# Performance work log

Measured on AMD Instinct MI355X. Metric: run time of the kernel, lower is better.

The kernel has to match this reference:

```python
import jax, jax.numpy as jnp
import numpy as np

E = 200      # embsize
R = 480      # num relations
T = 8        # cur_ts (history length)
N = 40000    # num entities
B = 1024     # batch of triples
NEG_INF = -1.0e9


def _lin(x, W, b):
    # torch nn.Linear convention: y = x @ W.T + b
    return x @ W.T + b


def _gru_cell(x, h, wih, whh, bih, bhh):
    # torch GRUCell: gates packed as [r, z, n]
    gi = x @ wih.T + bih
    gh = h @ whh.T + bhh
    i_r, i_z, i_n = jnp.split(gi, 3, axis=1)
    h_r, h_z, h_n = jnp.split(gh, 3, axis=1)
    r = jax.nn.sigmoid(i_r + h_r)
    z = jax.nn.sigmoid(i_z + h_z)
    n = jnp.tanh(i_n + r * h_n)
    return (1.0 - z) * n + z * h


def setup_inputs() -> dict:
    key = jax.random.key(0)
    ks = jax.random.split(key, 24)
    s = 0.05
    pre_emb = jax.random.normal(ks[0], (N, E), dtype=jnp.float32)
    r_emb = jax.random.normal(ks[1], (R, E), dtype=jnp.float32)
    partial_embeding = jax.random.randint(ks[2], (B, T * R), 0, 2).astype(jnp.float32)
    sub = jax.random.randint(ks[3], (B,), 0, N)
    rel = jax.random.randint(ks[4], (B,), 0, R)
    obj = jax.random.randint(ks[5], (B,), 0, N)
    all_triples = jnp.stack([sub, rel, obj], axis=1).astype(jnp.int64)
    params = {
        'W1': jax.random.normal(ks[6], (2 * E, E)) * s, 'b1': jnp.zeros((2 * E,)),
        'W2': jax.random.normal(ks[7], (E, 2 * E)) * s, 'b2': jnp.zeros((E,)),
        'Wa': jax.random.normal(ks[8], (E, E)) * s, 'ba': jnp.zeros((E,)),
        'Wh1': jax.random.normal(ks[9], (E, E)) * s, 'bh1': jnp.zeros((E,)),
        'Wh2': jax.random.normal(ks[10], (E, E)) * s, 'bh2': jnp.zeros((E,)),
        'Wal': jax.random.normal(ks[11], (E, E)) * s, 'bal': jnp.zeros((E,)),
        'gru_wih': jax.random.normal(ks[12], (3 * E, E)) * s,
        'gru_whh': jax.random.normal(ks[13], (3 * E, E)) * s,
        'gru_bih': jnp.zeros((3 * E,)),
        'gru_bhh': jnp.zeros((3 * E,)),
    }
    params = {k: v.astype(jnp.float32) for k, v in params.items()}
    out = {'pre_emb': pre_emb, 'r_emb': r_emb, 'partial_embeding': partial_embeding,
           'all_triples': all_triples, 'cur_ts': T, 'num_rel': R}
    out.update(params)
    return out


def reference(pre_emb, r_emb, partial_embeding, all_triples, cur_ts, num_rel,
              W1, b1, W2, b2, Wa, ba, Wh1, bh1, Wh2, bh2, Wal, bal,
              gru_wih, gru_whh, gru_bih, gru_bhh):
    mapped_rel = _lin(_lin(r_emb, W1, b1), W2, b2)          # [R, E]
    q_rel = mapped_rel[all_triples[:, 1]]                    # [B, E]
    b = partial_embeding.shape[0]

    # loop-invariant attention base: linear_attn(q_rel) @ mapped_rel^T -> [B, R]
    base = _lin(q_rel, Wa, ba) @ mapped_rel.T

    # [B, cur_ts*R] -> [cur_ts, B, R] for scan over timesteps
    pe = partial_embeding.reshape(b, cur_ts, num_rel).transpose(1, 0, 2)

    def step(h, cur):
        attn = cur * base
        attn = jnp.where(attn == 0, jnp.float32(NEG_INF), attn)
        a = jax.nn.softmax(attn, axis=1)
        x = a @ mapped_rel                                   # [B, E]
        h = _gru_cell(x, h, gru_wih, gru_whh, gru_bih, gru_bhh)
        return h, None

    h0 = jnp.zeros((b, mapped_rel.shape[1]), dtype=pre_emb.dtype)
    gru_hidden, _ = jax.lax.scan(step, h0, pe)

    predicted_hist = 0.1 * _lin(_lin(q_rel, Wh1, bh1), Wh2, bh2) + q_rel
    match_loss = jnp.mean((predicted_hist - gru_hidden) ** 2)

    # forward_forth (distmult scoring)
    gru_hidden2 = _gru_cell(q_rel, predicted_hist, gru_wih, gru_whh, gru_bih, gru_bhh)
    sub_emb = pre_emb[all_triples[:, 0]]
    score_logits = (_lin(sub_emb, Wal, bal) * gru_hidden2) @ _lin(pre_emb, Wal, bal).T  # [B, N]
    score = jax.nn.sigmoid(score_logits)

    labels = jnp.zeros_like(score_logits).at[jnp.arange(b), all_triples[:, 2]].set(1.0)
    # stable BCE(sigmoid(s), y)
    path_loss = -jnp.mean(labels * jax.nn.log_sigmoid(score_logits)
                          + (1.0 - labels) * jax.nn.log_sigmoid(-score_logits))
    return (match_loss, path_loss, score)
```

## Files before the change

### kernel.cpp

```cpp
#include <hip/hip_runtime.h>
#include <hip/hip_bf16.h>
#include <math.h>

#define EE 200
#define RR 480
#define TT 8
#define NN 40000
#define BB 1024
#define KP 224
#define GP 672
#define GPR 704
#define LDS_STRIDE 232

typedef __attribute__((ext_vector_type(8))) short short8v;
typedef __attribute__((ext_vector_type(4))) float f32x4;

__device__ inline unsigned short f2bf(float x) {
    unsigned int u = __float_as_uint(x);
    unsigned int r = ((u >> 16) & 1u) + 0x7fffu;
    return (unsigned short)((u + r) >> 16);
}
__device__ inline float bf2f(unsigned short h) {
    return __uint_as_float(((unsigned int)h) << 16);
}
__device__ inline float sigm(float x) { return 1.0f / (1.0f + __expf(-x)); }
__device__ inline void split_store(unsigned short* hi, unsigned short* lo, size_t i, float v) {
    unsigned short h = f2bf(v);
    hi[i] = h;
    lo[i] = f2bf(v - bf2f(h));
}

struct PrepPtrs {
    unsigned short *W1h, *W1l, *W2h, *W2l, *Wabh, *Wabl, *Wh2h, *Wh2l;
    unsigned short *Walh, *Wall, *WTh, *WTl, *wgh, *wgl, *whg, *whl;
    float *bab, *bihp, *bhhp;
    unsigned short *mapSh, *mapSl, *wgiSh, *wgiSl, *hbufs;
    double* acc;
};

__global__ __launch_bounds__(256) void prep_kernel(
    const float* __restrict__ W1, const float* __restrict__ W2,
    const float* __restrict__ Wa, const float* __restrict__ Wh1,
    const float* __restrict__ Wh2, const float* __restrict__ Wal,
    const float* __restrict__ bal, const float* __restrict__ wih,
    const float* __restrict__ whh, const float* __restrict__ ba,
    const float* __restrict__ bh1, const float* __restrict__ bih,
    const float* __restrict__ bhh, PrepPtrs p)
{
    const int gt = blockIdx.x * 256 + threadIdx.x;
    const int gs = gridDim.x * 256;

    for (int i = gt; i < 448 * 224; i += gs) {
        int r = i / 224, c = i - r * 224;
        split_store(p.W1h, p.W1l, i, (r < 400 && c < 200) ? W1[r * 200 + c] : 0.f);
        float vab = 0.f;
        if (c < 200) {
            if (r < 200) vab = Wa[r * 200 + c];
            else if (r >= 224 && r < 424) vab = Wh1[(r - 224) * 200 + c];
        }
        split_store(p.Wabh, p.Wabl, i, vab);
    }
    for (int i = gt; i < 256 * 416; i += gs) {
        int r = i / 416, c = i - r * 416;
        split_store(p.W2h, p.W2l, i, (r < 200 && c < 400) ? W2[r * 400 + c] : 0.f);
    }
    for (int i = gt; i < 256 * 224; i += gs) {
        int r = i / 224, c = i - r * 224;
        bool in = (r < 200 && c < 200);
        split_store(p.Wh2h, p.Wh2l, i, in ? Wh2[r * 200 + c] : 0.f);
        split_store(p.Walh, p.Wall, i, in ? Wal[r * 200 + c] : 0.f);
        float vt = in ? Wal[c * 200 + r] : ((r == 200 && c < 200) ? bal[c] : 0.f);
        split_store(p.WTh, p.WTl, i, vt);
    }
    for (int i = gt; i < 672 * 224; i += gs) {
        int rr = i / 224, c = i - rr * 224;
        int g = rr / 224, j = rr - g * 224;
        bool in = (j < 200 && c < 200);
        split_store(p.wgh, p.wgl, i, in ? wih[(size_t)(g * 200 + j) * 200 + c] : 0.f);
        split_store(p.whg, p.whl, i, in ? whh[(size_t)(g * 200 + j) * 200 + c] : 0.f);
    }
    for (int i = gt; i < 448; i += gs) {
        float v = 0.f;
        if (i < 200) v = ba[i];
        else if (i >= 224 && i < 424) v = bh1[i - 224];
        p.bab[i] = v;
    }
    for (int i = gt; i < GPR; i += gs) {
        int g = i / 224, j = i - g * 224;
        p.bihp[i] = (g < 3 && j < 200) ? bih[g * 200 + j] : 0.f;
    }
    for (int i = gt; i < GP; i += gs) {
        int g = i / 224, j = i - g * 224;
        p.bhhp[i] = (j < 200) ? bhh[g * 200 + j] : 0.f;
    }
    for (int i = gt; i < 512 * 224; i += gs) { p.mapSh[i] = 0; p.mapSl[i] = 0; }
    for (int i = gt; i < 704 * 480; i += gs) { p.wgiSh[i] = 0; p.wgiSl[i] = 0; }
    for (int i = gt; i < 4 * BB * KP; i += gs) p.hbufs[i] = 0;
    if (gt == 0) { p.acc[0] = 0.0; p.acc[1] = 0.0; }
}

template <int MODE, int OUT, int GATHER, int GATEPAD, int EGATHER>
__global__ __launch_bounds__(256) void mfma_flyA(
    const float* __restrict__ A, int lda, const int* __restrict__ gidx, int gsel,
    const unsigned short* __restrict__ Bhi, const unsigned short* __restrict__ Blo,
    const float* __restrict__ bias,
    float* __restrict__ Cf, unsigned short* __restrict__ Chi, unsigned short* __restrict__ Clo,
    int M, int N, int Ka, int Ks,
    const float* __restrict__ extra, int eld, float alpha, int obf)
{
    const int tid = threadIdx.x;
    const int wave = tid >> 6, lane = tid & 63;
    const int r16 = lane & 15, kq = lane >> 4;
    const int kbase = kq * 8;
    const int bm = blockIdx.y * 64 + wave * 16;
    const int bn = blockIdx.x * 64;

    int arow = bm + r16;
    const bool avalid = arow < M;
    if (GATHER) { if (avalid) arow = gidx[arow * 3 + gsel]; }
    const float* Ap = A + (size_t)arow * lda;

    f32x4 acc[4] = {{0,0,0,0},{0,0,0,0},{0,0,0,0},{0,0,0,0}};
    const int nk = Ks >> 5;

    for (int kk = 0; kk < nk; kk++) {
        const int k0 = kk * 32 + kbase;
        short8v a0, a1;
        #pragma unroll
        for (int e = 0; e < 8; e++) {
            float v = (avalid && (k0 + e) < Ka) ? Ap[k0 + e] : 0.f;
            unsigned short h = f2bf(v);
            a0[e] = (short)h;
            a1[e] = (short)f2bf(v - bf2f(h));
        }
        #pragma unroll
        for (int nf = 0; nf < 4; nf++) {
            const size_t boff = (size_t)(bn + nf * 16 + r16) * Ks + k0;
            short8v b0 = *(const short8v*)(Bhi + boff);
            short8v b1 = *(const short8v*)(Blo + boff);
            acc[nf] = __builtin_amdgcn_mfma_f32_16x16x32_bf16(a0, b1, acc[nf], 0, 0, 0);
            acc[nf] = __builtin_amdgcn_mfma_f32_16x16x32_bf16(a1, b0, acc[nf], 0, 0, 0);
            acc[nf] = __builtin_amdgcn_mfma_f32_16x16x32_bf16(a0, b0, acc[nf], 0, 0, 0);
        }
    }

    #pragma unroll
    for (int r = 0; r < 4; r++) {
        const int orow = bm + kq * 4 + r;
        if (orow >= M) continue;
        #pragma unroll
        for (int nf = 0; nf < 4; nf++) {
            const int col = bn + nf * 16 + r16;
            float v = acc[nf][r];
            if (OUT == 0) {
                if (col < N) {
                    if (bias) v += bias[col];
                    if (MODE == 1) {
                        float ex = EGATHER ? extra[(size_t)gidx[orow * 3 + gsel] * eld + col]
                                           : extra[(size_t)orow * eld + col];
                        v = alpha * v + ex;
                    } else if (MODE == 2) {
                        v = v * extra[(size_t)orow * eld + col];
                    }
                    Cf[(size_t)orow * N + col] = v;
                }
            } else if (OUT == 1) {
                if (col < obf) {
                    float w = 0.f;
                    if (col < N) { w = v; if (bias) w += bias[col]; }
                    Chi[(size_t)orow * obf + col] = f2bf(w);
                }
            } else if (OUT == 2) {
                if (col < N) {
                    int wr = GATEPAD ? (orow / 200) * 224 + orow % 200 : orow;
                    if (bias) v += bias[col];
                    split_store(Chi, Clo, (size_t)wr * obf + col, v);
                }
            } else if (OUT == 3) {
                if (col < N) {
                    if (bias) v += bias[col];
                    Cf[(size_t)orow * N + col] = v;
                    split_store(Chi, Clo, (size_t)orow * obf + col, v);
                }
            }
        }
    }
}

__global__ __launch_bounds__(256) void mfma_linear1_kernel(
    const unsigned short* __restrict__ Ahi,
    const unsigned short* __restrict__ Bhi,
    const float* __restrict__ bias, float* __restrict__ C,
    int M, int N, int Ks)
{
    const int tid  = threadIdx.x;
    const int wave = tid >> 6;
    const int lane = tid & 63;
    const int r16   = lane & 15;
    const int khalf = lane >> 4;
    const int kbase = khalf * 8;
    const int bm = blockIdx.y * 64 + wave * 16;
    const int bn = blockIdx.x * 64;

    const unsigned short* ah = Ahi + (size_t)(bm + r16) * Ks + kbase;
    const unsigned short* bh = Bhi + (size_t)(bn + r16) * Ks + kbase;

    f32x4 acc[4] = {{0,0,0,0},{0,0,0,0},{0,0,0,0},{0,0,0,0}};

    for (int k0 = 0; k0 < Ks; k0 += 32) {
        short8v a0 = *(const short8v*)(ah + k0);
        #pragma unroll
        for (int nf = 0; nf < 4; nf++) {
            short8v b0 = *(const short8v*)(bh + (size_t)nf * 16 * Ks + k0);
            acc[nf] = __builtin_amdgcn_mfma_f32_16x16x32_bf16(a0, b0, acc[nf], 0, 0, 0);
        }
    }
    #pragma unroll
    for (int r = 0; r < 4; r++) {
        const int row = bm + khalf * 4 + r;
        #pragma unroll
        for (int nf = 0; nf < 4; nf++) {
            const int col = bn + nf * 16 + r16;
            if (col < N)
                C[(size_t)row * N + col] = acc[nf][r] + (bias ? bias[col] : 0.0f);
        }
    }
}

template <int FIRST, int LAST>
__global__ __launch_bounds__(256) void gru_step_kernel(
    const unsigned short* __restrict__ Whi, const unsigned short* __restrict__ Wlo,
    const float* __restrict__ bhh_pad,
    const float* __restrict__ gi_t,
    const unsigned short* __restrict__ hin_hi, const unsigned short* __restrict__ hin_lo,
    unsigned short* __restrict__ hout_hi, unsigned short* __restrict__ hout_lo,
    float* __restrict__ h_fin)
{
    const int tid = threadIdx.x;
    const int wave = tid >> 6, lane = tid & 63;
    const int r16 = lane & 15, kq = lane >> 4;
    const int jf = blockIdx.x;
    const int brow = (blockIdx.y * 4 + wave) * 16;
    const int j = jf * 16 + r16;

    f32x4 ar = {0,0,0,0}, az = {0,0,0,0}, an = {0,0,0,0};
    if (!FIRST) {
        short8v ahi[7], alo[7];
        const unsigned short* hh = hin_hi + (size_t)(brow + r16) * KP + kq * 8;
        const unsigned short* hl = hin_lo + (size_t)(brow + r16) * KP + kq * 8;
        #pragma unroll
        for (int kk = 0; kk < 7; kk++) {
            ahi[kk] = *(const short8v*)(hh + kk * 32);
            alo[kk] = *(const short8v*)(hl + kk * 32);
        }
        #pragma unroll
        for (int kk = 0; kk < 7; kk++) {
            const size_t rowr = (size_t)(jf * 16 + r16) * KP + kk * 32 + kq * 8;
            const size_t rowz = rowr + (size_t)224 * KP;
            const size_t rown = rowr + (size_t)448 * KP;
            short8v brh = *(const short8v*)(Whi + rowr);
            short8v brl = *(const short8v*)(Wlo + rowr);
            short8v bzh = *(const short8v*)(Whi + rowz);
            short8v bzl = *(const short8v*)(Wlo + rowz);
            short8v bnh = *(const short8v*)(Whi + rown);
            short8v bnl = *(const short8v*)(Wlo + rown);
            ar = __builtin_amdgcn_mfma_f32_16x16x32_bf16(ahi[kk], brl, ar, 0, 0, 0);
            az = __builtin_amdgcn_mfma_f32_16x16x32_bf16(ahi[kk], bzl, az, 0, 0, 0);
            an = __builtin_amdgcn_mfma_f32_16x16x32_bf16(ahi[kk], bnl, an, 0, 0, 0);
            ar = __builtin_amdgcn_mfma_f32_16x16x32_bf16(alo[kk], brh, ar, 0, 0, 0);
            az = __builtin_amdgcn_mfma_f32_16x16x32_bf16(alo[kk], bzh, az, 0, 0, 0);
            an = __builtin_amdgcn_mfma_f32_16x16x32_bf16(alo[kk], bnh, an, 0, 0, 0);
            ar = __builtin_amdgcn_mfma_f32_16x16x32_bf16(ahi[kk], brh, ar, 0, 0, 0);
            az = __builtin_amdgcn_mfma_f32_16x16x32_bf16(ahi[kk], bzh, az, 0, 0, 0);
            an = __builtin_amdgcn_mfma_f32_16x16x32_bf16(ahi[kk], bnh, an, 0, 0, 0);
        }
    }

    const float br = bhh_pad[j], bz = bhh_pad[224 + j], bn_ = bhh_pad[448 + j];
    #pragma unroll
    for (int q = 0; q < 4; q++) {
        const int row = brow + kq * 4 + q;
        float gir = gi_t[(size_t)row * GP + j];
        float giz = gi_t[(size_t)row * GP + 224 + j];
        float gin = gi_t[(size_t)row * GP + 448 + j];
        float r_ = sigm(gir + ar[q] + br);
        float z_ = sigm(giz + az[q] + bz);
        float n_ = tanhf(gin + r_ * (an[q] + bn_));
        float hold = 0.0f;
        if (!FIRST)
            hold = bf2f(hin_hi[(size_t)row * KP + j]) + bf2f(hin_lo[(size_t)row * KP + j]);
        float hnew = (1.0f - z_) * n_ + z_ * hold;
        if (j < EE) {
            unsigned short nh = f2bf(hnew);
            hout_hi[(size_t)row * KP + j] = nh;
            hout_lo[(size_t)row * KP + j] = f2bf(hnew - bf2f(nh));
            if (LAST) h_fin[(size_t)row * EE + j] = hnew;
        }
    }
}

__global__ __launch_bounds__(256) void gru2_fused_kernel(
    const unsigned short* __restrict__ Wihi, const unsigned short* __restrict__ Wilo,
    const unsigned short* __restrict__ Whhi, const unsigned short* __restrict__ Whlo,
    const float* __restrict__ bih_pad, const float* __restrict__ bhh_pad,
    const int* __restrict__ triples, const float* __restrict__ map,
    const float* __restrict__ hp, const float* __restrict__ hfin,
    float* __restrict__ ghid2, double* __restrict__ accMatch)
{
    __shared__ float red[256];
    const int tid = threadIdx.x;
    const int wave = tid >> 6, lane = tid & 63;
    const int r16 = lane & 15, kq = lane >> 4;
    const int jf = blockIdx.x;
    const int brow = (blockIdx.y * 4 + wave) * 16;
    const int j = jf * 16 + r16;

    f32x4 ir = {0,0,0,0}, iz = {0,0,0,0}, in_ = {0,0,0,0};
    f32x4 hr = {0,0,0,0}, hz = {0,0,0,0}, hn = {0,0,0,0};

    {
        const int xrow = triples[(brow + r16) * 3 + 1];
        const float* xp = map + (size_t)xrow * EE;
        #pragma unroll
        for (int kk = 0; kk < 7; kk++) {
            short8v a0, a1;
            #pragma unroll
            for (int e = 0; e < 8; e++) {
                int k = kk * 32 + kq * 8 + e;
                float v = (k < EE) ? xp[k] : 0.0f;
                unsigned short hhh = f2bf(v);
                a0[e] = (short)hhh;
                a1[e] = (short)f2bf(v - bf2f(hhh));
            }
            const size_t rowr = (size_t)(jf * 16 + r16) * KP + kk * 32 + kq * 8;
            const size_t rowz = rowr + (size_t)224 * KP;
            const size_t rown = rowr + (size_t)448 * KP;
            short8v brh = *(const short8v*)(Wihi + rowr);
            short8v brl = *(const short8v*)(Wilo + rowr);
            short8v bzh = *(const short8v*)(Wihi + rowz);
            short8v bzl = *(const short8v*)(Wilo + rowz);
            short8v bnh = *(const short8v*)(Wihi + rown);
            short8v bnl = *(const short8v*)(Wilo + rown);
            ir = __builtin_amdgcn_mfma_f32_16x16x32_bf16(a0, brl, ir, 0, 0, 0);
            iz = __builtin_amdgcn_mfma_f32_16x16x32_bf16(a0, bzl, iz, 0, 0, 0);
            in_ = __builtin_amdgcn_mfma_f32_16x16x32_bf16(a0, bnl, in_, 0, 0, 0);
            ir = __builtin_amdgcn_mfma_f32_16x16x32_bf16(a1, brh, ir, 0, 0, 0);
            iz = __builtin_amdgcn_mfma_f32_16x16x32_bf16(a1, bzh, iz, 0, 0, 0);
            in_ = __builtin_amdgcn_mfma_f32_16x16x32_bf16(a1, bnh, in_, 0, 0, 0);
            ir = __builtin_amdgcn_mfma_f32_16x16x32_bf16(a0, brh, ir, 0, 0, 0);
            iz = __builtin_amdgcn_mfma_f32_16x16x32_bf16(a0, bzh, iz, 0, 0, 0);
            in_ = __builtin_amdgcn_mfma_f32_16x16x32_bf16(a0, bnh, in_, 0, 0, 0);
        }
    }
    {
        const float* hpp = hp + (size_t)(brow + r16) * EE;
        #pragma unroll
        for (int kk = 0; kk < 7; kk++) {
            short8v a0, a1;
            #pragma unroll
            for (int e = 0; e < 8; e++) {
                int k = kk * 32 + kq * 8 + e;
                float v = (k < EE) ? hpp[k] : 0.0f;
                unsigned short hhh = f2bf(v);
                a0[e] = (short)hhh;
                a1[e] = (short)f2bf(v - bf2f(hhh));
            }
            const size_t rowr = (size_t)(jf * 16 + r16) * KP + kk * 32 + kq * 8;
            const size_t rowz = rowr + (size_t)224 * KP;
            const size_t rown = rowr + (size_t)448 * KP;
            short8v brh = *(const short8v*)(Whhi + rowr);
            short8v brl = *(const short8v*)(Whlo + rowr);
            short8v bzh = *(const short8v*)(Whhi + rowz);
            short8v bzl = *(const short8v*)(Whlo + rowz);
            short8v bnh = *(const short8v*)(Whhi + rown);
            short8v bnl = *(const short8v*)(Whlo + rown);
            hr = __builtin_amdgcn_mfma_f32_16x16x32_bf16(a0, brl, hr, 0, 0, 0);
            hz = __builtin_amdgcn_mfma_f32_16x16x32_bf16(a0, bzl, hz, 0, 0, 0);
            hn = __builtin_amdgcn_mfma_f32_16x16x32_bf16(a0, bnl, hn, 0, 0, 0);
            hr = __builtin_amdgcn_mfma_f32_16x16x32_bf16(a1, brh, hr, 0, 0, 0);
            hz = __builtin_amdgcn_mfma_f32_16x16x32_bf16(a1, bzh, hz, 0, 0, 0);
            hn = __builtin_amdgcn_mfma_f32_16x16x32_bf16(a1, bnh, hn, 0, 0, 0);
            hr = __builtin_amdgcn_mfma_f32_16x16x32_bf16(a0, brh, hr, 0, 0, 0);
            hz = __builtin_amdgcn_mfma_f32_16x16x32_bf16(a0, bzh, hz, 0, 0, 0);
            hn = __builtin_amdgcn_mfma_f32_16x16x32_bf16(a0, bnh, hn, 0, 0, 0);
        }
    }

    float psum = 0.0f;
    if (j < EE) {
        const float bir = bih_pad[j], biz = bih_pad[224 + j], bin = bih_pad[448 + j];
        const float bhr = bhh_pad[j], bhz = bhh_pad[224 + j], bhn = bhh_pad[448 + j];
        #pragma unroll
        for (int q = 0; q < 4; q++) {
            const int row = brow + kq * 4 + q;
            float r_ = sigm(ir[q] + bir + hr[q] + bhr);
            float z_ = sigm(iz[q] + biz + hz[q] + bhz);
            float n_ = tanhf(in_[q] + bin + r_ * (hn[q] + bhn));
            float hold = hp[(size_t)row * EE + j];
            ghid2[(size_t)row * EE + j] = (1.0f - z_) * n_ + z_ * hold;
            float d = hold - hfin[(size_t)row * EE + j];
            psum += d * d;
        }
    }
    red[tid] = psum;
    __syncthreads();
    for (int s = 128; s > 0; s >>= 1) {
        if (tid < s) red[tid] += red[tid + s];
        __syncthreads();
    }
    if (tid == 0) atomicAdd(accMatch, (double)red[0]);
}

__global__ __launch_bounds__(256) void score_mfma2_kernel(
    const unsigned short* __restrict__ Ubf,
    const float* __restrict__ pre_emb,
    const int* __restrict__ triples,
    float* __restrict__ outScore,
    double* __restrict__ accPath)
{
    __shared__ unsigned short Bs[32 * LDS_STRIDE];
    __shared__ int objs[BB];
    __shared__ float red[256];

    const int tid = threadIdx.x;
    const int bn = blockIdx.x * 32;

    for (int i = tid; i < BB; i += 256) objs[i] = triples[i * 3 + 2];

    for (int idx = tid; idx < 32 * 50; idx += 256) {
        int row = idx / 50;
        int c4 = (idx - row * 50) * 4;
        float4 v = *(const float4*)(pre_emb + (size_t)(bn + row) * EE + c4);
        unsigned short* d = &Bs[row * LDS_STRIDE + c4];
        d[0] = f2bf(v.x); d[1] = f2bf(v.y); d[2] = f2bf(v.z); d[3] = f2bf(v.w);
    }
    for (int idx = tid; idx < 32 * 24; idx += 256) {
        int row = idx / 24;
        int cc = idx - row * 24;
        Bs[row * LDS_STRIDE + 200 + cc] = (cc == 0) ? (unsigned short)0x3F80 : (unsigned short)0;
    }
    __syncthreads();

    const int wave  = tid >> 6;
    const int lane  = tid & 63;
    const int r16   = lane & 15;
    const int khalf = lane >> 4;
    const int kbase = khalf * 8;

    short8v b0r[7], b1r[7];
    #pragma unroll
    for (int kk = 0; kk < 7; kk++) {
        b0r[kk] = *(const short8v*)&Bs[( 0 + r16) * LDS_STRIDE + kk * 32 + kbase];
        b1r[kk] = *(const short8v*)&Bs[(16 + r16) * LDS_STRIDE + kk * 32 + kbase];
    }

    float psum = 0.0f;

    for (int mi = 0; mi < 16; mi++) {
        const int m0 = mi * 64 + wave * 16;
        const unsigned short* Ap = Ubf + (size_t)(m0 + r16) * KP + kbase;
        f32x4 acc0 = {0,0,0,0}, acc1 = {0,0,0,0};
        #pragma unroll
        for (int kk = 0; kk < 7; kk++) {
            short8v a = *(const short8v*)(Ap + kk * 32);
            acc0 = __builtin_amdgcn_mfma_f32_16x16x32_bf16(a, b0r[kk], acc0, 0, 0, 0);
            acc1 = __builtin_amdgcn_mfma_f32_16x16x32_bf16(a, b1r[kk], acc1, 0, 0, 0);
        }
        #pragma unroll
        for (int r = 0; r < 4; r++) {
            const int grow = m0 + khalf * 4 + r;
            const int objc = objs[grow];
            float xv[2] = { acc0[r], acc1[r] };
            #pragma unroll
            for (int nf = 0; nf < 2; nf++) {
                const int col = bn + nf * 16 + r16;
                float x  = xv[nf];
                float e  = __expf(-fabsf(x));
                float t1 = 1.0f + e;
                float rc = __builtin_amdgcn_rcpf(t1);
                float sig = (x >= 0.0f) ? rc : e * rc;
                float sp = __logf(t1);
                float s  = (col == objc) ? x : -x;
                psum += fminf(s, 0.0f) - sp;
                outScore[(size_t)grow * NN + col] = sig;
            }
        }
    }
    red[tid] = psum;
    __syncthreads();
    for (int s = 128; s > 0; s >>= 1) {
        if (tid < s) red[tid] += red[tid + s];
        __syncthreads();
    }
    if (tid == 0) atomicAdd(accPath, (double)red[0]);
}

__global__ __launch_bounds__(256) void masked_softmax_all_kernel(
    const float* __restrict__ base, const float* __restrict__ part,
    unsigned short* __restrict__ aout_hi)
{
    __shared__ float sv[RR];
    __shared__ float red[256];
    const int blk = blockIdx.x;
    const int b = blk & (BB - 1);
    const int t = blk >> 10;
    const int tid = threadIdx.x;
    const float* brow = base + (size_t)b * RR;
    const float* prow = part + (size_t)b * (TT * RR) + t * RR;

    float lmax = -3.0e38f;
    for (int r = tid; r < RR; r += 256) {
        float v = prow[r] * brow[r];
        if (v == 0.0f) v = -1000000000.0f;
        sv[r] = v;
        lmax = fmaxf(lmax, v);
    }
    red[tid] = lmax;
    __syncthreads();
    for (int s = 128; s > 0; s >>= 1) {
        if (tid < s) red[tid] = fmaxf(red[tid], red[tid + s]);
        __syncthreads();
    }
    float gmax = red[0];
    __syncthreads();

    float lsum = 0.0f;
    for (int r = tid; r < RR; r += 256) {
        float e = __expf(sv[r] - gmax);
        sv[r] = e;
        lsum += e;
    }
    red[tid] = lsum;
    __syncthreads();
    for (int s = 128; s > 0; s >>= 1) {
        if (tid < s) red[tid] += red[tid + s];
        __syncthreads();
    }
    float inv = 1.0f / red[0];
    for (int r = tid; r < RR; r += 256)
        aout_hi[(size_t)blk * RR + r] = f2bf(sv[r] * inv);
}

__global__ void final_kernel(const double* __restrict__ acc, float* __restrict__ out)
{
    if (threadIdx.x == 0) {
        out[0] = (float)(acc[0] / ((double)BB * EE));
        out[1] = (float)(-acc[1] / ((double)BB * NN));
    }
}

extern "C" void kernel_launch(void* const* d_in, const int* in_sizes, int n_in,
                              void* d_out, int out_size, void* d_ws, size_t ws_size,
                              hipStream_t stream) {
    const float* pre_emb = (const float*)d_in[0];
    const float* r_emb   = (const float*)d_in[1];
    const float* part    = (const float*)d_in[2];
    const int*   triples = (const int*)d_in[3];
    const float* W1  = (const float*)d_in[6];
    const float* b1  = (const float*)d_in[7];
    const float* W2  = (const float*)d_in[8];
    const float* b2  = (const float*)d_in[9];
    const float* Wa  = (const float*)d_in[10];
    const float* ba  = (const float*)d_in[11];
    const float* Wh1 = (const float*)d_in[12];
    const float* bh1 = (const float*)d_in[13];
    const float* Wh2 = (const float*)d_in[14];
    const float* bh2 = (const float*)d_in[15];
    const float* Wal = (const float*)d_in[16];
    const float* bal = (const float*)d_in[17];
    const float* wih = (const float*)d_in[18];
    const float* whh = (const float*)d_in[19];
    const float* bih = (const float*)d_in[20];
    const float* bhh = (const float*)d_in[21];

    float* out = (float*)d_out;
    double* acc = (double*)d_ws;
    float* wsf = (float*)d_ws;
    size_t off = 4;
    auto alloc = [&](size_t n) { float* p = wsf + off; off += (n + 3) & ~(size_t)3; return p; };
    auto allocS = [&](size_t n) { return (unsigned short*)alloc((n + 1) / 2); };

    PrepPtrs p;
    p.W1h  = allocS((size_t)448 * 224);
    p.W1l  = allocS((size_t)448 * 224);
    p.W2h  = allocS((size_t)256 * 416);
    p.W2l  = allocS((size_t)256 * 416);
    p.Wabh = allocS((size_t)448 * 224);
    p.Wabl = allocS((size_t)448 * 224);
    p.Wh2h = allocS((size_t)256 * 224);
    p.Wh2l = allocS((size_t)256 * 224);
    p.Walh = allocS((size_t)256 * 224);
    p.Wall = allocS((size_t)256 * 224);
    p.WTh  = allocS((size_t)256 * 224);
    p.WTl  = allocS((size_t)256 * 224);
    p.wgh  = allocS((size_t)GP * KP);
    p.wgl  = allocS((size_t)GP * KP);
    p.whg  = allocS((size_t)GP * KP);
    p.whl  = allocS((size_t)GP * KP);
    p.bab  = alloc(448);
    p.bihp = alloc(GPR);
    p.bhhp = alloc(GP);
    p.mapSh = allocS((size_t)512 * 224);
    p.mapSl = allocS((size_t)512 * 224);
    p.wgiSh = allocS((size_t)GPR * RR);
    p.wgiSl = allocS((size_t)GPR * RR);
    p.hbufs = allocS((size_t)4 * BB * KP);
    p.acc = acc;

    unsigned short* ha_hi = p.hbufs;
    unsigned short* ha_lo = p.hbufs + (size_t)BB * KP;
    unsigned short* hb_hi = p.hbufs + (size_t)2 * BB * KP;
    unsigned short* hb_lo = p.hbufs + (size_t)3 * BB * KP;

    float* h1     = alloc((size_t)RR * 400);
    float* map    = alloc((size_t)RR * EE);
    float* qa_ph1 = alloc((size_t)BB * 448);
    float* basep  = alloc((size_t)BB * RR);
    unsigned short* aw_hi = allocS((size_t)TT * BB * RR);
    float* gi_all = alloc((size_t)TT * BB * GP);
    float* hfin   = alloc((size_t)BB * EE);
    float* pred   = alloc((size_t)BB * EE);
    float* ghid2  = alloc((size_t)BB * EE);
    float* s1h    = alloc((size_t)BB * EE);
    unsigned short* u_bf = allocS((size_t)BB * KP);

    dim3 blk(256);

    prep_kernel<<<1024, blk, 0, stream>>>(
        W1, W2, Wa, Wh1, Wh2, Wal, bal, wih, whh, ba, bh1, bih, bhh, p);

    mfma_flyA<0,0,0,0,0><<<dim3(7, 8), blk, 0, stream>>>(
        r_emb, 200, nullptr, 0, p.W1h, p.W1l, b1, h1, nullptr, nullptr,
        RR, 400, 200, 224, nullptr, 0, 0.f, 0);
    mfma_flyA<0,3,0,0,0><<<dim3(4, 8), blk, 0, stream>>>(
        h1, 400, nullptr, 0, p.W2h, p.W2l, b2, map, p.mapSh, p.mapSl,
        RR, EE, 400, 416, nullptr, 0, 0.f, 224);
    mfma_flyA<0,0,1,0,0><<<dim3(7, 16), blk, 0, stream>>>(
        map, 200, triples, 1, p.Wabh, p.Wabl, p.bab, qa_ph1, nullptr, nullptr,
        BB, 448, 200, 224, nullptr, 0, 0.f, 0);
    mfma_flyA<0,0,0,0,0><<<dim3(8, 16), blk, 0, stream>>>(
        qa_ph1, 448, nullptr, 0, p.mapSh, p.mapSl, nullptr, basep, nullptr, nullptr,
        BB, RR, 200, 224, nullptr, 0, 0.f, 0);
    masked_softmax_all_kernel<<<TT * BB, blk, 0, stream>>>(basep, part, aw_hi);
    mfma_flyA<0,2,0,1,0><<<dim3(8, 10), blk, 0, stream>>>(
        wih, 200, nullptr, 0, p.mapSh, p.mapSl, nullptr, nullptr, p.wgiSh, p.wgiSl,
        600, RR, 200, 224, nullptr, 0, 0.f, RR);
    mfma_linear1_kernel<<<dim3(11, TT * BB / 64), blk, 0, stream>>>(
        aw_hi, p.wgiSh, p.bihp, gi_all, TT * BB, GP, RR);

    for (int t = 0; t < TT; t++) {
        const float* gi_t = gi_all + (size_t)t * BB * GP;
        const unsigned short* ih = (t & 1) ? hb_hi : ha_hi;
        const unsigned short* il = (t & 1) ? hb_lo : ha_lo;
        unsigned short* oh = (t & 1) ? ha_hi : hb_hi;
        unsigned short* ol = (t & 1) ? ha_lo : hb_lo;
        if (t == 0)
            gru_step_kernel<1,0><<<dim3(13, BB / 64), blk, 0, stream>>>(
                p.whg, p.whl, p.bhhp, gi_t, ih, il, oh, ol, nullptr);
        else if (t == TT - 1)
            gru_step_kernel<0,1><<<dim3(13, BB / 64), blk, 0, stream>>>(
                p.whg, p.whl, p.bhhp, gi_t, ih, il, oh, ol, hfin);
        else
            gru_step_kernel<0,0><<<dim3(13, BB / 64), blk, 0, stream>>>(
                p.whg, p.whl, p.bhhp, gi_t, ih, il, oh, ol, nullptr);
    }

    mfma_flyA<1,0,0,0,1><<<dim3(4, 16), blk, 0, stream>>>(
        qa_ph1 + 224, 448, triples, 1, p.Wh2h, p.Wh2l, bh2, pred, nullptr, nullptr,
        BB, EE, 200, 224, map, 200, 0.1f, 0);
    gru2_fused_kernel<<<dim3(13, BB / 64), blk, 0, stream>>>(
        p.wgh, p.wgl, p.whg, p.whl, p.bihp, p.bhhp,
        triples, map, pred, hfin, ghid2, acc + 0);
    mfma_flyA<2,0,1,0,0><<<dim3(4, 16), blk, 0, stream>>>(
        pre_emb, 200, triples, 0, p.Walh, p.Wall, bal, s1h, nullptr, nullptr,
        BB, EE, 200, 224, ghid2, 200, 0.f, 0);
    mfma_flyA<0,1,0,0,0><<<dim3(4, 16), blk, 0, stream>>>(
        s1h, 200, nullptr, 0, p.WTh, p.WTl, nullptr, nullptr, u_bf, nullptr,
        BB, KP, 200, 224, nullptr, 0, 0.f, KP);
    score_mfma2_kernel<<<NN / 32, blk, 0, stream>>>(u_bf, pre_emb, triples, out + 2, acc + 1);
    final_kernel<<<1, 64, 0, stream>>>(acc, out);
}
```

Before: 400.5 us.

## Restructure score GEMM grid to keep A fragments in registers and stream entity tiles

```diff
diff --git a/kernel.cpp b/kernel.cpp
--- a/kernel.cpp
+++ b/kernel.cpp
@@ -11,6 +11,7 @@
 #define GP 672
 #define GPR 704
 #define LDS_STRIDE 232
+#define SPAN 800
 
 typedef __attribute__((ext_vector_type(8))) short short8v;
 typedef __attribute__((ext_vector_type(4))) float f32x4;
@@ -411,7 +412,7 @@
     if (tid == 0) atomicAdd(accMatch, (double)red[0]);
 }
 
-__global__ __launch_bounds__(256) void score_mfma2_kernel(
+__global__ __launch_bounds__(256) void score_mfma3_kernel(
     const unsigned short* __restrict__ Ubf,
     const float* __restrict__ pre_emb,
     const int* __restrict__ triples,
@@ -419,57 +420,57 @@
     double* __restrict__ accPath)
 {
     __shared__ unsigned short Bs[32 * LDS_STRIDE];
-    __shared__ int objs[BB];
+    __shared__ int objs[64];
     __shared__ float red[256];
 
     const int tid = threadIdx.x;
-    const int bn = blockIdx.x * 32;
-
-    for (int i = tid; i < BB; i += 256) objs[i] = triples[i * 3 + 2];
-
-    for (int idx = tid; idx < 32 * 50; idx += 256) {
-        int row = idx / 50;
-        int c4 = (idx - row * 50) * 4;
-        float4 v = *(const float4*)(pre_emb + (size_t)(bn + row) * EE + c4);
-        unsigned short* d = &Bs[row * LDS_STRIDE + c4];
-        d[0] = f2bf(v.x); d[1] = f2bf(v.y); d[2] = f2bf(v.z); d[3] = f2bf(v.w);
-    }
+    const int wave = tid >> 6, lane = tid & 63;
+    const int r16 = lane & 15, khalf = lane >> 4;
+    const int kbase = khalf * 8;
+    const int colbase = blockIdx.x * SPAN;
+    const int mbase = blockIdx.y * 64;
+    const int m0 = mbase + wave * 16;
+
+    if (tid < 64) objs[tid] = triples[(mbase + tid) * 3 + 2];
     for (int idx = tid; idx < 32 * 24; idx += 256) {
         int row = idx / 24;
         int cc = idx - row * 24;
         Bs[row * LDS_STRIDE + 200 + cc] = (cc == 0) ? (unsigned short)0x3F80 : (unsigned short)0;
     }
-    __syncthreads();
-
-    const int wave  = tid >> 6;
-    const int lane  = tid & 63;
-    const int r16   = lane & 15;
-    const int khalf = lane >> 4;
-    const int kbase = khalf * 8;
-
-    short8v b0r[7], b1r[7];
-    #pragma unroll
-    for (int kk = 0; kk < 7; kk++) {
-        b0r[kk] = *(const short8v*)&Bs[( 0 + r16) * LDS_STRIDE + kk * 32 + kbase];
-        b1r[kk] = *(const short8v*)&Bs[(16 + r16) * LDS_STRIDE + kk * 32 + kbase];
+
+    short8v a[7];
+    {
+        const unsigned short* Ap = Ubf + (size_t)(m0 + r16) * KP + kbase;
+        #pragma unroll
+        for (int kk = 0; kk < 7; kk++) a[kk] = *(const short8v*)(Ap + kk * 32);
     }
 
     float psum = 0.0f;
 
-    for (int mi = 0; mi < 16; mi++) {
-        const int m0 = mi * 64 + wave * 16;
-        const unsigned short* Ap = Ubf + (size_t)(m0 + r16) * KP + kbase;
+    for (int cj = 0; cj < SPAN / 32; cj++) {
+        const int bn = colbase + cj * 32;
+        __syncthreads();
+        for (int idx = tid; idx < 32 * 50; idx += 256) {
+            int row = idx / 50;
+            int c4 = (idx - row * 50) * 4;
+            float4 v = *(const float4*)(pre_emb + (size_t)(bn + row) * EE + c4);
+            unsigned short* d = &Bs[row * LDS_STRIDE + c4];
+            d[0] = f2bf(v.x); d[1] = f2bf(v.y); d[2] = f2bf(v.z); d[3] = f2bf(v.w);
+        }
+        __syncthreads();
+
         f32x4 acc0 = {0,0,0,0}, acc1 = {0,0,0,0};
         #pragma unroll
         for (int kk = 0; kk < 7; kk++) {
-            short8v a = *(const short8v*)(Ap + kk * 32);
-            acc0 = __builtin_amdgcn_mfma_f32_16x16x32_bf16(a, b0r[kk], acc0, 0, 0, 0);
-            acc1 = __builtin_amdgcn_mfma_f32_16x16x32_bf16(a, b1r[kk], acc1, 0, 0, 0);
+            short8v b0 = *(const short8v*)&Bs[( 0 + r16) * LDS_STRIDE + kk * 32 + kbase];
+            short8v b1 = *(const short8v*)&Bs[(16 + r16) * LDS_STRIDE + kk * 32 + kbase];
+            acc0 = __builtin_amdgcn_mfma_f32_16x16x32_bf16(a[kk], b0, acc0, 0, 0, 0);
+            acc1 = __builtin_amdgcn_mfma_f32_16x16x32_bf16(a[kk], b1, acc1, 0, 0, 0);
         }
         #pragma unroll
         for (int r = 0; r < 4; r++) {
             const int grow = m0 + khalf * 4 + r;
-            const int objc = objs[grow];
+            const int objc = objs[grow - mbase];
             float xv[2] = { acc0[r], acc1[r] };
             #pragma unroll
             for (int nf = 0; nf < 2; nf++) {
@@ -677,6 +678,6 @@
     mfma_flyA<0,1,0,0,0><<<dim3(4, 16), blk, 0, stream>>>(
         s1h, 200, nullptr, 0, p.WTh, p.WTl, nullptr, nullptr, u_bf, nullptr,
         BB, KP, 200, 224, nullptr, 0, 0.f, KP);
-    score_mfma2_kernel<<<NN / 32, blk, 0, stream>>>(u_bf, pre_emb, triples, out + 2, acc + 1);
+    score_mfma3_kernel<<<dim3(50, 16), blk, 0, stream>>>(u_bf, pre_emb, triples, out + 2, acc + 1);
     final_kernel<<<1, 64, 0, stream>>>(acc, out);
 }
```

Measured after the change: 457.2 us. 1.14x slower.
